# Kernel tuning notes

Measured on AMD Instinct MI355X. Metric: run time of the kernel, lower is better.

Reference implementation:

```python
import jax, jax.numpy as jnp
import numpy as np

B, S, HIDDEN = 2, 2048, 1024
NUM_HEADS, HEAD_DIM = 16, 64
STRIDE = 128
NEG = -10000.0


def _strided_mask(seq_len):
    # Sparse Transformer strided pattern: causal, local window of STRIDE,
    # plus every STRIDE-th previous position.
    i = jnp.arange(seq_len)[:, None]
    j = jnp.arange(seq_len)[None, :]
    diff = i - j
    allowed = (diff >= 0) & ((diff < STRIDE) | (diff % STRIDE == 0))
    return jnp.where(allowed, 0.0, NEG).astype(jnp.float32)  # [S, S]


def setup_inputs() -> dict:
    key = jax.random.key(0)
    k0, k1, k2, k3, k4 = jax.random.split(key, 5)
    hidden_states = jax.random.normal(k0, (B, S, HIDDEN), dtype=jnp.float32)
    attention_mask = jnp.zeros((B, 1, 1, S), dtype=jnp.float32)
    W_q = jax.random.normal(k1, (HIDDEN, HIDDEN), dtype=jnp.float32) * 0.02
    b_q = jnp.zeros((HIDDEN,), dtype=jnp.float32)
    W_v = jax.random.normal(k2, (HIDDEN, HIDDEN), dtype=jnp.float32) * 0.02
    b_v = jnp.zeros((HIDDEN,), dtype=jnp.float32)
    return {"hidden_states": hidden_states, "attention_mask": attention_mask,
            "W_q": W_q, "b_q": b_q, "W_v": W_v, "b_v": b_v}


def _heads(x):
    b, s, _ = x.shape
    return x.reshape(b, s, NUM_HEADS, HEAD_DIM).transpose(0, 2, 1, 3)  # [B,H,S,d]


def reference(hidden_states, attention_mask, W_q, b_q, W_v, b_v):
    q = _heads(hidden_states @ W_q + b_q)  # [B,H,S,d]
    v = _heads(hidden_states @ W_v + b_v)  # [B,H,S,d]
    hash_mask = _strided_mask(q.shape[-2])  # [S,S], broadcast over B,H
    # NB: source computes matmul(query, query^T) -- Q used for both sides.
    scores = jnp.einsum('bhid,bhjd->bhij', q, q) + hash_mask
    scores = scores / jnp.sqrt(jnp.asarray(HEAD_DIM, scores.dtype))
    scores = scores + attention_mask
    probs = jax.nn.softmax(scores, axis=-1)  # dropout p=0 (eval)
    ctx = jnp.einsum('bhij,bhjd->bhid', probs, v)  # [B,H,S,d]
    b = ctx.shape[0]
    return ctx.transpose(0, 2, 1, 3).reshape(b, -1, NUM_HEADS * HEAD_DIM)
```

## Files before the change

### kernel.cpp

```cpp
#include <hip/hip_runtime.h>

typedef __attribute__((ext_vector_type(8))) short short8;
typedef __attribute__((ext_vector_type(4))) float float4v;

__device__ inline float bf2f(ushort u) {
    unsigned v = ((unsigned)u) << 16;
    return __builtin_bit_cast(float, v);
}
__device__ inline ushort f2bf(float f) {
    unsigned u = __builtin_bit_cast(unsigned, f);
    u += 0x7FFFu + ((u >> 16) & 1u);
    return (ushort)(u >> 16);
}

__device__ inline void gload_lds16(const ushort* g, ushort* l) {
    __builtin_amdgcn_global_load_lds(
        (const __attribute__((address_space(1))) unsigned int*)g,
        (__attribute__((address_space(3))) unsigned int*)l,
        16, 0, 0);
}

__global__ __launch_bounds__(256) void prep(
    const float* __restrict__ hs, ushort* __restrict__ hsb,
    const float* __restrict__ Wq, const float* __restrict__ Wv,
    ushort* __restrict__ Wt) {
    __shared__ ushort tile[64][68];
    if (blockIdx.x < 1024) {
        const size_t base = ((size_t)blockIdx.x * 256 + threadIdx.x) * 16;
        union { ushort u[16]; uint4 v[2]; } o;
#pragma unroll
        for (int q = 0; q < 4; ++q) {
            float4v f = *(const float4v*)(hs + base + q * 4);
#pragma unroll
            for (int j = 0; j < 4; ++j) o.u[q * 4 + j] = f2bf(f[j]);
        }
        *(uint4*)(hsb + base)     = o.v[0];
        *(uint4*)(hsb + base + 8) = o.v[1];
        return;
    }
    const int idx = blockIdx.x - 1024;
    const int z = idx >> 8, yy = (idx >> 4) & 15, xx = idx & 15;
    const float* W = z ? Wv : Wq;
    ushort* Wto    = Wt + (z ? (size_t)1024 * 1024 : 0);
    const int k0 = yy * 64, n0 = xx * 64;
    const int tid = threadIdx.x;
    const int rr = tid >> 4;
    const int cc = (tid & 15) * 4;
    union U4 { ushort u[4]; uint2 v; };
#pragma unroll
    for (int i = 0; i < 4; ++i) {
        int row = rr + i * 16;
        float4v f = *(const float4v*)(W + (size_t)(k0 + row) * 1024 + n0 + cc);
        U4 x;
#pragma unroll
        for (int j = 0; j < 4; ++j) x.u[j] = f2bf(f[j]);
        *(uint2*)&tile[row][cc] = x.v;
    }
    __syncthreads();
#pragma unroll
    for (int i = 0; i < 4; ++i) {
        int row = rr + i * 16;
        U4 o;
#pragma unroll
        for (int j = 0; j < 4; ++j) o.u[j] = tile[cc + j][row];
        *(uint2*)(Wto + (size_t)(n0 + row) * 1024 + k0 + cc) = o.v;
    }
}

__global__ __launch_bounds__(512, 2) void qv_gemm(
    const ushort* __restrict__ hsb, const ushort* __restrict__ Wt,
    const float* __restrict__ bq, const float* __restrict__ bv,
    ushort* __restrict__ q_ws, ushort* __restrict__ v_ws) {
    __shared__ ushort smem[73728];
    const int wg = blockIdx.x;
    const int n0 = (wg & 7) * 256;
    const int m0 = (wg >> 3) * 128;
    const int tid  = threadIdx.x;
    const int wid  = tid >> 6, lane = tid & 63;
    const int quad = lane >> 4, l16 = lane & 15;
    const int wm = (wid >> 2) * 64;
    const int wn = (wid & 3) * 64;
    const int srow8 = tid >> 3;
    const int scb   = (tid & 7) * 16;

    auto stage = [&](int ktt, int bi, int r) {
        if (r < 2) {
            int row = r * 64 + srow8;
            int sb  = scb ^ ((row & 7) << 4);
            gload_lds16(hsb + (size_t)(m0 + row) * 1024 + ktt * 64 + (sb >> 1),
                        (ushort*)((char*)smem + bi * 49152 + r * 8192 + wid * 1024));
        } else {
            int row = (r - 2) * 64 + srow8;
            int sb  = scb ^ ((row & 7) << 4);
            gload_lds16(Wt + (size_t)(n0 + row) * 1024 + ktt * 64 + (sb >> 1),
                        (ushort*)((char*)smem + bi * 49152 + 16384 + (r - 2) * 8192 + wid * 1024));
        }
    };

    float4v acc[4][4] = {};

#pragma unroll
    for (int r = 0; r < 6; ++r) stage(0, 0, r);
#pragma unroll
    for (int r = 0; r < 6; ++r) stage(1, 1, r);

    int bi = 0;
    for (int ktt = 0; ktt < 16; ++ktt) {
        const char* Ab = (const char*)smem + bi * 49152;
        const char* Bb = Ab + 16384;

        if (ktt < 15) asm volatile("s_waitcnt vmcnt(6)" ::: "memory");
        else          asm volatile("s_waitcnt vmcnt(0)" ::: "memory");
        __builtin_amdgcn_s_barrier();
        __builtin_amdgcn_sched_barrier(0);

        short8 af[4][2], bfr[4][2];
#pragma unroll
        for (int mt = 0; mt < 4; ++mt) {
            int ar = wm + mt * 16 + l16;
            int sw = (ar & 7) << 4;
            af[mt][0] = *(const short8*)(Ab + ar * 128 + ((quad * 16) ^ sw));
        }
#pragma unroll
        for (int nt = 0; nt < 4; ++nt) {
            int br = wn + nt * 16 + l16;
            int sw = (br & 7) << 4;
            bfr[nt][0] = *(const short8*)(Bb + br * 128 + ((quad * 16) ^ sw));
        }
        __builtin_amdgcn_sched_barrier(0);
        const int kn = ktt + 2;
        const int b2 = (bi + 2 >= 3) ? bi - 1 : bi + 2;
        if (kn < 16) {
            stage(kn, b2, 0); stage(kn, b2, 1); stage(kn, b2, 2);
            stage(kn, b2, 3); stage(kn, b2, 4); stage(kn, b2, 5);
        }
#pragma unroll
        for (int mt = 0; mt < 4; ++mt) {
            int ar = wm + mt * 16 + l16;
            int sw = (ar & 7) << 4;
            af[mt][1] = *(const short8*)(Ab + ar * 128 + (((4 + quad) * 16) ^ sw));
        }
#pragma unroll
        for (int nt = 0; nt < 4; ++nt) {
            int br = wn + nt * 16 + l16;
            int sw = (br & 7) << 4;
            bfr[nt][1] = *(const short8*)(Bb + br * 128 + (((4 + quad) * 16) ^ sw));
        }
        __builtin_amdgcn_sched_barrier(0);
        asm volatile("s_waitcnt lgkmcnt(8)" ::: "memory");
        __builtin_amdgcn_sched_barrier(0);
        __builtin_amdgcn_s_setprio(1);
#pragma unroll
        for (int mt = 0; mt < 4; ++mt)
#pragma unroll
            for (int nt = 0; nt < 4; ++nt)
                acc[mt][nt] = __builtin_amdgcn_mfma_f32_16x16x32_bf16(
                    af[mt][0], bfr[nt][0], acc[mt][nt], 0, 0, 0);
        __builtin_amdgcn_s_setprio(0);
        asm volatile("s_waitcnt lgkmcnt(0)" ::: "memory");
        __builtin_amdgcn_sched_barrier(0);
        __builtin_amdgcn_s_setprio(1);
#pragma unroll
        for (int mt = 0; mt < 4; ++mt)
#pragma unroll
            for (int nt = 0; nt < 4; ++nt)
                acc[mt][nt] = __builtin_amdgcn_mfma_f32_16x16x32_bf16(
                    af[mt][1], bfr[nt][1], acc[mt][nt], 0, 0, 0);
        __builtin_amdgcn_s_setprio(0);

        bi = (bi + 1 >= 3) ? 0 : bi + 1;
    }

#pragma unroll
    for (int mt = 0; mt < 4; ++mt) {
#pragma unroll
        for (int nt = 0; nt < 4; ++nt) {
            int coln = n0 + wn + nt * 16 + l16;
            bool isq = coln < 1024;
            int c2 = isq ? coln : coln - 1024;
            float bsv = isq ? bq[c2] : bv[c2];
            ushort* outp = isq ? q_ws : v_ws;
            int hh = c2 >> 6, dd = c2 & 63;
#pragma unroll
            for (int reg = 0; reg < 4; ++reg) {
                int r = m0 + wm + mt * 16 + quad * 4 + reg;
                int bb = r >> 11, s = r & 2047;
                outp[(((size_t)bb * 16 + hh) * 2048 + s) * 64 + dd] =
                    f2bf(acc[mt][nt][reg] + bsv);
            }
        }
    }
}

#define SISSUE(As, Bs, Ms, idx) { const ushort* kr_ = q_ws + srbase + ((size_t)(idx) << 13); \
    As = *(const uint4*)kr_; Bs = *(const uint4*)(kr_ + 8); Ms = amask[amrow + ((idx) << 7)]; }
#define SCONS(As, Bs, Ms, kk) { union { uint4 v; ushort u[8]; } t0_, t1_; t0_.v = As; t1_.v = Bs; \
    float p_ = 0.f; \
    _Pragma("unroll") for (int jj = 0; jj < 8; ++jj) p_ += qv[jj] * bf2f(t0_.u[jj]); \
    _Pragma("unroll") for (int jj = 0; jj < 8; ++jj) p_ += qv[8 + jj] * bf2f(t1_.u[jj]); \
    p_ += __shfl_xor(p_, 1); p_ += __shfl_xor(p_, 2); \
    if ((tid & 3) == 0) Sstr[sr][kk] = p_ * 0.125f + Ms; }
#define VISSUE(As, Bs, idx) { const ushort* vr_ = v_ws + srbase + ((size_t)(idx) << 13); \
    As = *(const uint4*)vr_; Bs = *(const uint4*)(vr_ + 8); }
#define VCONS(As, Bs, kk) { float p_ = Sstr[sr][kk]; union { uint4 v; ushort u[8]; } t0_, t1_; \
    t0_.v = As; t1_.v = Bs; \
    _Pragma("unroll") for (int jj = 0; jj < 8; ++jj) acc16[jj] += p_ * bf2f(t0_.u[jj]); \
    _Pragma("unroll") for (int jj = 0; jj < 8; ++jj) acc16[8 + jj] += p_ * bf2f(t1_.u[jj]); }

__global__ __launch_bounds__(512, 4) void attn(
    const ushort* __restrict__ q_ws, const ushort* __restrict__ v_ws,
    const float* __restrict__ amask, float* __restrict__ out) {
    const int wg = blockIdx.x;
    const int lane8 = wg & 7;
    const int k8    = wg >> 3;
    const int kk    = k8 & 31, khalf = k8 >> 5;
    const int t  = khalf ? (15 - (kk & 15)) : (kk & 15);
    const int gq = (kk >> 4) + 2 * khalf;
    const int g  = gq * 8 + lane8;
    const int b  = g >> 4;
    const int h  = g & 15;

    __shared__ ushort KwPl[16384];
    __shared__ ushort VtS[16384];
    __shared__ float  Sstr[128][17];
    __shared__ float  amw[256];

    const int tid = threadIdx.x;
    const int wid = tid >> 6, lane = tid & 63;
    const int quad = lane >> 4, l16 = lane & 15;
    const int r0 = wid * 16;
    const size_t qbase = ((size_t)b * 16 + h) * 2048 * 64;
    const int base_row = (t - 1) * 128;
    const int nk = (t >= 2) ? (t - 1) : 0;

    const int sr = tid >> 2;
    const int dq = (tid & 3) * 16;
    const size_t srbase = qbase + (size_t)sr * 64 + dq;
    const size_t amrow  = (size_t)b * 2048 + sr;

#pragma unroll
    for (int i = 0; i < 4; ++i) {
        int u = tid + i * 512;
        int row = u >> 3, c = u & 7;
        int jg = base_row + row; if (jg < 0) jg = 0;
        int sc = c ^ (row & 7);
        gload_lds16(q_ws + qbase + (size_t)jg * 64 + sc * 8, &KwPl[u * 8]);
    }
    __builtin_amdgcn_sched_barrier(0);

    {
        const int vj = tid & 255, dh0 = (tid >> 8) * 32;
        int vjg = base_row + vj; if (vjg < 0) vjg = 0;
        const ushort* vsrc = v_ws + qbase + (size_t)vjg * 64 + dh0;
        int cj = vj >> 3, j7 = vj & 7;
#pragma unroll
        for (int d0 = 0; d0 < 32; d0 += 8) {
            union { uint4 v; ushort u[8]; } tmp;
            tmp.v = *(const uint4*)(vsrc + d0);
#pragma unroll
            for (int jj = 0; jj < 8; ++jj) {
                int dd = dh0 + d0 + jj;
                VtS[dd * 256 + ((cj ^ (dd & 7)) * 8) + j7] = tmp.u[jj];
            }
        }
        int amj = base_row + (tid & 255); if (amj < 0) amj = 0;
        amw[tid & 255] = amask[(size_t)b * 2048 + amj];
    }

    uint4 kA0{}, kB0{}, kA1{}, kB1{}, kA2{}, kB2{};
    float am0 = 0.f, am1 = 0.f, am2 = 0.f;
    if (nk > 0) {
        SISSUE(kA0, kB0, am0, 0);
        SISSUE(kA1, kB1, am1, (1 < nk ? 1 : 0));
        SISSUE(kA2, kB2, am2, (2 < nk ? 2 : 0));
    }

    asm volatile("s_waitcnt vmcnt(0) lgkmcnt(0)" ::: "memory");
    __builtin_amdgcn_s_barrier();
    __builtin_amdgcn_sched_barrier(0);

    if (nk > 0) {
        float qv[16];
#pragma unroll
        for (int cc = 0; cc < 2; ++cc) {
            int c = (dq >> 3) + cc;
            union { uint4 v; ushort u[8]; } tm;
            tm.v = *(const uint4*)&KwPl[(128 + sr) * 64 + ((c ^ (sr & 7)) * 8)];
#pragma unroll
            for (int jj = 0; jj < 8; ++jj) qv[cc * 8 + jj] = bf2f(tm.u[jj]);
        }
        for (int k = 0; k < nk; k += 3) {
            SCONS(kA0, kB0, am0, k);
            if (k + 3 < nk) SISSUE(kA0, kB0, am0, k + 3);
            if (k + 1 < nk) {
                SCONS(kA1, kB1, am1, k + 1);
                if (k + 4 < nk) SISSUE(kA1, kB1, am1, k + 4);
            }
            if (k + 2 < nk) {
                SCONS(kA2, kB2, am2, k + 2);
                if (k + 5 < nk) SISSUE(kA2, kB2, am2, k + 5);
            }
        }
    }

    float4v sacc[16] = {};
    __builtin_amdgcn_s_setprio(1);
#pragma unroll
    for (int ks = 0; ks < 2; ++ks) {
        int c = ks * 4 + quad;
        int sw = (c ^ (l16 & 7)) * 8;
        short8 af = *(const short8*)&KwPl[(128 + r0 + l16) * 64 + sw];
#pragma unroll
        for (int nt = 0; nt < 16; ++nt) {
            short8 bfr = *(const short8*)&KwPl[(nt * 16 + l16) * 64 + sw];
            sacc[nt] = __builtin_amdgcn_mfma_f32_16x16x32_bf16(af, bfr, sacc[nt], 0, 0, 0);
        }
    }
    __builtin_amdgcn_s_setprio(0);
    __syncthreads();

    unsigned pb[4][4];
#pragma unroll
    for (int reg = 0; reg < 4; ++reg) {
        int rr = r0 + quad * 4 + reg;
        float sstr_v = (l16 < nk) ? Sstr[rr][l16] : -INFINITY;
        float m = sstr_v;
#pragma unroll
        for (int nt = 0; nt < 16; ++nt) {
            int c = nt * 16 + l16;
            bool allowed = (c >= rr) && (c <= rr + 128) && (t > 0 || c >= 128);
            float x = allowed ? sacc[nt][reg] * 0.125f + amw[c] : -INFINITY;
            sacc[nt][reg] = x;
            m = fmaxf(m, x);
        }
#pragma unroll
        for (int off = 1; off < 16; off <<= 1) m = fmaxf(m, __shfl_xor(m, off));

        float es = (l16 < nk) ? __expf(sstr_v - m) : 0.f;
        float sum = es;
#pragma unroll
        for (int nt = 0; nt < 16; ++nt) {
            float x = sacc[nt][reg];
            float e = (x == -INFINITY) ? 0.f : __expf(x - m);
            sacc[nt][reg] = e; sum += e;
        }
#pragma unroll
        for (int off = 1; off < 16; off <<= 1) sum += __shfl_xor(sum, off);
        float rden = 1.f / sum;
#pragma unroll
        for (int nt = 0; nt < 8; ++nt) {
            int c = nt * 2 + (l16 >> 3);
            KwPl[rr * 128 + ((c ^ (rr & 15)) * 8) + (l16 & 7)] = f2bf(sacc[nt][reg] * rden);
        }
#pragma unroll
        for (int i2 = 0; i2 < 4; ++i2) {
            unsigned lo = f2bf(sacc[8 + 2 * i2][reg] * rden);
            unsigned hi = f2bf(sacc[9 + 2 * i2][reg] * rden);
            pb[reg][i2] = lo | (hi << 16);
        }
        if (l16 < nk) Sstr[rr][l16] = es * rden;
    }
    __syncthreads();

    uint4 vA0{}, vB0{}, vA1{}, vB1{}, vA2{}, vB2{};
    if (nk > 0) {
        VISSUE(vA0, vB0, 0);
        VISSUE(vA1, vB1, (1 < nk ? 1 : 0));
        VISSUE(vA2, vB2, (2 < nk ? 2 : 0));
    }

    float4v cacc[4] = {};
    __builtin_amdgcn_s_setprio(1);
#pragma unroll
    for (int ks = 0; ks < 4; ++ks) {
        int cp = ks * 4 + quad;
        short8 af = *(const short8*)&KwPl[(r0 + l16) * 128 + ((cp ^ l16) * 8)];
#pragma unroll
        for (int nt = 0; nt < 4; ++nt) {
            int sw = (cp ^ (l16 & 7)) * 8;
            short8 bfr = *(const short8*)&VtS[(nt * 16 + l16) * 256 + sw];
            cacc[nt] = __builtin_amdgcn_mfma_f32_16x16x32_bf16(af, bfr, cacc[nt], 0, 0, 0);
        }
    }
    __builtin_amdgcn_s_setprio(0);
    __syncthreads();

#pragma unroll
    for (int reg = 0; reg < 4; ++reg) {
        int rr = r0 + quad * 4 + reg;
#pragma unroll
        for (int i2 = 0; i2 < 4; ++i2) {
            int nt0 = 8 + 2 * i2;
#pragma unroll
            for (int e2 = 0; e2 < 2; ++e2) {
                int nt = nt0 + e2;
                int c = (nt - 8) * 2 + (l16 >> 3);
                ushort val = (ushort)((pb[reg][i2] >> (16 * e2)) & 0xFFFF);
                KwPl[rr * 128 + ((c ^ (rr & 15)) * 8) + (l16 & 7)] = val;
            }
        }
    }
    __syncthreads();

    __builtin_amdgcn_s_setprio(1);
#pragma unroll
    for (int ks = 0; ks < 4; ++ks) {
        int cp = ks * 4 + quad;
        short8 af = *(const short8*)&KwPl[(r0 + l16) * 128 + ((cp ^ l16) * 8)];
#pragma unroll
        for (int nt = 0; nt < 4; ++nt) {
            int cv = 16 + cp;
            int sw = (cv ^ (l16 & 7)) * 8;
            short8 bfr = *(const short8*)&VtS[(nt * 16 + l16) * 256 + sw];
            cacc[nt] = __builtin_amdgcn_mfma_f32_16x16x32_bf16(af, bfr, cacc[nt], 0, 0, 0);
        }
    }
    __builtin_amdgcn_s_setprio(0);

    float acc16[16] = {};
    if (nk > 0) {
        for (int k = 0; k < nk; k += 3) {
            VCONS(vA0, vB0, k);
            if (k + 3 < nk) VISSUE(vA0, vB0, k + 3);
            if (k + 1 < nk) {
                VCONS(vA1, vB1, k + 1);
                if (k + 4 < nk) VISSUE(vA1, vB1, k + 4);
            }
            if (k + 2 < nk) {
                VCONS(vA2, vB2, k + 2);
                if (k + 5 < nk) VISSUE(vA2, vB2, k + 5);
            }
        }
    }
    __syncthreads();

    float* ctxp = (float*)&VtS[0];
#pragma unroll
    for (int d4 = 0; d4 < 4; ++d4) {
        int c = (dq >> 2) + d4;
        *(float4v*)&ctxp[sr * 64 + ((c ^ (sr & 15)) * 4)] =
            *(const float4v*)&acc16[d4 * 4];
    }
    __syncthreads();

    const size_t obase = ((size_t)b * 2048 + (size_t)t * 128) * 1024 + (size_t)h * 64;
#pragma unroll
    for (int nt = 0; nt < 4; ++nt)
#pragma unroll
        for (int reg = 0; reg < 4; ++reg) {
            int rr = r0 + quad * 4 + reg;
            int d = nt * 16 + l16;
            float cstr = ctxp[rr * 64 + (((d >> 2) ^ (rr & 15)) * 4) + (d & 3)];
            out[obase + (size_t)rr * 1024 + d] = cacc[nt][reg] + cstr;
        }
}

extern "C" void kernel_launch(void* const* d_in, const int* in_sizes, int n_in,
                              void* d_out, int out_size, void* d_ws, size_t ws_size,
                              hipStream_t stream) {
    int ihs = -1, iam = -1, iw1 = -1, iw2 = -1, ib1 = -1, ib2 = -1;
    for (int i = 0; i < n_in; ++i) {
        int s = in_sizes[i];
        if      (s == 4194304) { if (ihs < 0) ihs = i; }
        else if (s == 4096)    { if (iam < 0) iam = i; }
        else if (s == 1048576) { if (iw1 < 0) iw1 = i; else if (iw2 < 0) iw2 = i; }
        else if (s == 1024)    { if (ib1 < 0) ib1 = i; else if (ib2 < 0) ib2 = i; }
    }
    if (ihs < 0) ihs = 0; if (iam < 0) iam = 1;
    if (iw1 < 0) iw1 = 2; if (ib1 < 0) ib1 = 3;
    if (iw2 < 0) iw2 = 4; if (ib2 < 0) ib2 = 5;

    const float* hs    = (const float*)d_in[ihs];
    const float* amask = (const float*)d_in[iam];
    const float* Wq    = (const float*)d_in[iw1];
    const float* bq    = (const float*)d_in[ib1];
    const float* Wv    = (const float*)d_in[iw2];
    const float* bv    = (const float*)d_in[ib2];
    float* out = (float*)d_out;

    char* ws = (char*)d_ws;
    ushort* Wt   = (ushort*)(ws);
    ushort* hsb  = (ushort*)(ws + (1u << 22));
    ushort* q_ws = (ushort*)(ws + (1u << 22) + (1u << 23));
    ushort* v_ws = (ushort*)(ws + (1u << 22) + (2u << 23));

    prep<<<1536, 256, 0, stream>>>(hs, hsb, Wq, Wv, Wt);
    qv_gemm<<<256, 512, 0, stream>>>(hsb, Wt, bq, bv, q_ws, v_ws);
    attn<<<512, 512, 0, stream>>>(q_ws, v_ws, amask, out);
}
```

Before: 131.7 us.

## Split strided-attention part into separate kernel with partial softmax merge

Moves the strided (every-128th) key contributions out of the main attention kernel into a new sattn kernel. That kernel computes a per-row max, sum and unnormalized context for the strided keys from LDS-staged Q/V, and writes them to workspace. The main kernel then merges these partials with its local-window softmax using the combined max and a rescale factor. This removes the serial, latency-bound strided loop from the MFMA kernel and balances work across blocks. In exchange it adds an extra launch and a round trip of float context through global memory.

```diff
diff --git a/kernel.cpp b/kernel.cpp
--- a/kernel.cpp
+++ b/kernel.cpp
@@ -192,24 +192,104 @@
     }
 }
 
-#define SISSUE(As, Bs, Ms, idx) { const ushort* kr_ = q_ws + srbase + ((size_t)(idx) << 13); \
-    As = *(const uint4*)kr_; Bs = *(const uint4*)(kr_ + 8); Ms = amask[amrow + ((idx) << 7)]; }
-#define SCONS(As, Bs, Ms, kk) { union { uint4 v; ushort u[8]; } t0_, t1_; t0_.v = As; t1_.v = Bs; \
-    float p_ = 0.f; \
-    _Pragma("unroll") for (int jj = 0; jj < 8; ++jj) p_ += qv[jj] * bf2f(t0_.u[jj]); \
-    _Pragma("unroll") for (int jj = 0; jj < 8; ++jj) p_ += qv[8 + jj] * bf2f(t1_.u[jj]); \
-    p_ += __shfl_xor(p_, 1); p_ += __shfl_xor(p_, 2); \
-    if ((tid & 3) == 0) Sstr[sr][kk] = p_ * 0.125f + Ms; }
-#define VISSUE(As, Bs, idx) { const ushort* vr_ = v_ws + srbase + ((size_t)(idx) << 13); \
-    As = *(const uint4*)vr_; Bs = *(const uint4*)(vr_ + 8); }
-#define VCONS(As, Bs, kk) { float p_ = Sstr[sr][kk]; union { uint4 v; ushort u[8]; } t0_, t1_; \
-    t0_.v = As; t1_.v = Bs; \
-    _Pragma("unroll") for (int jj = 0; jj < 8; ++jj) acc16[jj] += p_ * bf2f(t0_.u[jj]); \
-    _Pragma("unroll") for (int jj = 0; jj < 8; ++jj) acc16[8 + jj] += p_ * bf2f(t1_.u[jj]); }
+__global__ __launch_bounds__(512, 4) void sattn(
+    const ushort* __restrict__ q_ws, const ushort* __restrict__ v_ws,
+    const float* __restrict__ amask, float* __restrict__ ctx_s,
+    float* __restrict__ msss) {
+    __shared__ ushort Qs[16][16][72];
+    __shared__ ushort Vs[16][16][72];
+    __shared__ float  am[16][16];
+    const int wg = blockIdx.x;
+    const int rg = wg & 7;
+    const int g  = wg >> 3;
+    const int b  = g >> 4;
+    const int tid = threadIdx.x;
+    const size_t gh = (size_t)g * 2048 * 64;
+    const int r0g = rg * 16;
+
+    {
+        int row = tid >> 1, half = tid & 1;
+        int m = row >> 4, res = row & 15;
+        int j = m * 128 + r0g + res;
+        const ushort* qsrc = q_ws + gh + (size_t)j * 64 + half * 32;
+        const ushort* vsrc = v_ws + gh + (size_t)j * 64 + half * 32;
+#pragma unroll
+        for (int c = 0; c < 4; ++c) {
+            *(uint4*)&Qs[m][res][half * 32 + c * 8] = *(const uint4*)(qsrc + c * 8);
+            *(uint4*)&Vs[m][res][half * 32 + c * 8] = *(const uint4*)(vsrc + c * 8);
+        }
+        if (tid < 256)
+            am[tid >> 4][tid & 15] =
+                amask[(size_t)b * 2048 + (tid >> 4) * 128 + r0g + (tid & 15)];
+    }
+    __syncthreads();
+
+    const int ti  = tid >> 5;
+    const int res = (tid >> 1) & 15;
+    const int dh  = tid & 1, d0 = dh * 32;
+    const int cnt = (ti >= 2) ? (ti - 1) : 0;
+
+    float q[32];
+#pragma unroll
+    for (int c = 0; c < 4; ++c) {
+        union { uint4 v; ushort u[8]; } tm;
+        tm.v = *(const uint4*)&Qs[ti][res][d0 + c * 8];
+#pragma unroll
+        for (int jj = 0; jj < 8; ++jj) q[c * 8 + jj] = bf2f(tm.u[jj]);
+    }
+
+    float m = -INFINITY;
+    for (int k = 0; k < cnt; ++k) {
+        float p = 0.f;
+#pragma unroll
+        for (int c = 0; c < 4; ++c) {
+            union { uint4 v; ushort u[8]; } tm;
+            tm.v = *(const uint4*)&Qs[k][res][d0 + c * 8];
+#pragma unroll
+            for (int jj = 0; jj < 8; ++jj) p += q[c * 8 + jj] * bf2f(tm.u[jj]);
+        }
+        p += __shfl_xor(p, 1);
+        m = fmaxf(m, p * 0.125f + am[k][res]);
+    }
+
+    float sum = 0.f;
+    float ctx[32] = {};
+    for (int k = 0; k < cnt; ++k) {
+        float p = 0.f;
+#pragma unroll
+        for (int c = 0; c < 4; ++c) {
+            union { uint4 v; ushort u[8]; } tm;
+            tm.v = *(const uint4*)&Qs[k][res][d0 + c * 8];
+#pragma unroll
+            for (int jj = 0; jj < 8; ++jj) p += q[c * 8 + jj] * bf2f(tm.u[jj]);
+        }
+        p += __shfl_xor(p, 1);
+        float e = __expf(p * 0.125f + am[k][res] - m);
+        sum += e;
+#pragma unroll
+        for (int c = 0; c < 4; ++c) {
+            union { uint4 v; ushort u[8]; } tv;
+            tv.v = *(const uint4*)&Vs[k][res][d0 + c * 8];
+#pragma unroll
+            for (int jj = 0; jj < 8; ++jj) ctx[c * 8 + jj] += e * bf2f(tv.u[jj]);
+        }
+    }
+
+    if (cnt > 0) {
+        int i = ti * 128 + r0g + res;
+        size_t rb = (size_t)g * 2048 + i;
+        if (dh == 0) { msss[rb * 2] = m; msss[rb * 2 + 1] = sum; }
+        float* cp = ctx_s + rb * 64 + d0;
+#pragma unroll
+        for (int c = 0; c < 8; ++c)
+            *(float4v*)(cp + c * 4) = *(const float4v*)&ctx[c * 4];
+    }
+}
 
 __global__ __launch_bounds__(512, 4) void attn(
     const ushort* __restrict__ q_ws, const ushort* __restrict__ v_ws,
-    const float* __restrict__ amask, float* __restrict__ out) {
+    const float* __restrict__ amask, const float* __restrict__ ctx_s,
+    const float* __restrict__ msss, float* __restrict__ out) {
     const int wg = blockIdx.x;
     const int lane8 = wg & 7;
     const int k8    = wg >> 3;
@@ -218,25 +298,19 @@
     const int gq = (kk >> 4) + 2 * khalf;
     const int g  = gq * 8 + lane8;
     const int b  = g >> 4;
-    const int h  = g & 15;
 
     __shared__ ushort KwPl[16384];
     __shared__ ushort VtS[16384];
-    __shared__ float  Sstr[128][17];
     __shared__ float  amw[256];
+    __shared__ float  msl[128][2];
+    __shared__ float  fsw[128];
 
     const int tid = threadIdx.x;
     const int wid = tid >> 6, lane = tid & 63;
     const int quad = lane >> 4, l16 = lane & 15;
     const int r0 = wid * 16;
-    const size_t qbase = ((size_t)b * 16 + h) * 2048 * 64;
+    const size_t qbase = (size_t)g * 2048 * 64;
     const int base_row = (t - 1) * 128;
-    const int nk = (t >= 2) ? (t - 1) : 0;
-
-    const int sr = tid >> 2;
-    const int dq = (tid & 3) * 16;
-    const size_t srbase = qbase + (size_t)sr * 64 + dq;
-    const size_t amrow  = (size_t)b * 2048 + sr;
 
 #pragma unroll
     for (int i = 0; i < 4; ++i) {
@@ -265,43 +339,20 @@
         }
         int amj = base_row + (tid & 255); if (amj < 0) amj = 0;
         amw[tid & 255] = amask[(size_t)b * 2048 + amj];
-    }
-
-    uint4 kA0{}, kB0{}, kA1{}, kB1{}, kA2{}, kB2{};
-    float am0 = 0.f, am1 = 0.f, am2 = 0.f;
-    if (nk > 0) {
-        SISSUE(kA0, kB0, am0, 0);
-        SISSUE(kA1, kB1, am1, (1 < nk ? 1 : 0));
-        SISSUE(kA2, kB2, am2, (2 < nk ? 2 : 0));
+        if (tid < 128) {
+            if (t >= 2) {
+                size_t rb = (size_t)g * 2048 + t * 128 + tid;
+                msl[tid][0] = msss[rb * 2];
+                msl[tid][1] = msss[rb * 2 + 1];
+            } else {
+                msl[tid][0] = -INFINITY; msl[tid][1] = 0.f;
+            }
+        }
     }
 
     asm volatile("s_waitcnt vmcnt(0) lgkmcnt(0)" ::: "memory");
     __builtin_amdgcn_s_barrier();
     __builtin_amdgcn_sched_barrier(0);
-
-    if (nk > 0) {
-        float qv[16];
-#pragma unroll
-        for (int cc = 0; cc < 2; ++cc) {
-            int c = (dq >> 3) + cc;
-            union { uint4 v; ushort u[8]; } tm;
-            tm.v = *(const uint4*)&KwPl[(128 + sr) * 64 + ((c ^ (sr & 7)) * 8)];
-#pragma unroll
-            for (int jj = 0; jj < 8; ++jj) qv[cc * 8 + jj] = bf2f(tm.u[jj]);
-        }
-        for (int k = 0; k < nk; k += 3) {
-            SCONS(kA0, kB0, am0, k);
-            if (k + 3 < nk) SISSUE(kA0, kB0, am0, k + 3);
-            if (k + 1 < nk) {
-                SCONS(kA1, kB1, am1, k + 1);
-                if (k + 4 < nk) SISSUE(kA1, kB1, am1, k + 4);
-            }
-            if (k + 2 < nk) {
-                SCONS(kA2, kB2, am2, k + 2);
-                if (k + 5 < nk) SISSUE(kA2, kB2, am2, k + 5);
-            }
-        }
-    }
 
     float4v sacc[16] = {};
     __builtin_amdgcn_s_setprio(1);
@@ -323,8 +374,8 @@
 #pragma unroll
     for (int reg = 0; reg < 4; ++reg) {
         int rr = r0 + quad * 4 + reg;
-        float sstr_v = (l16 < nk) ? Sstr[rr][l16] : -INFINITY;
-        float m = sstr_v;
+        float msv = msl[rr][0], ssv = msl[rr][1];
+        float m = -INFINITY;
 #pragma unroll
         for (int nt = 0; nt < 16; ++nt) {
             int c = nt * 16 + l16;
@@ -335,18 +386,20 @@
         }
 #pragma unroll
         for (int off = 1; off < 16; off <<= 1) m = fmaxf(m, __shfl_xor(m, off));
-
-        float es = (l16 < nk) ? __expf(sstr_v - m) : 0.f;
-        float sum = es;
+        float M = fmaxf(m, msv);
+
+        float sum = 0.f;
 #pragma unroll
         for (int nt = 0; nt < 16; ++nt) {
             float x = sacc[nt][reg];
-            float e = (x == -INFINITY) ? 0.f : __expf(x - m);
+            float e = (x == -INFINITY) ? 0.f : __expf(x - M);
             sacc[nt][reg] = e; sum += e;
         }
 #pragma unroll
         for (int off = 1; off < 16; off <<= 1) sum += __shfl_xor(sum, off);
-        float rden = 1.f / sum;
+
+        float fs = (t >= 2) ? __expf(msv - M) : 0.f;
+        float rden = 1.f / (sum + ssv * fs);
 #pragma unroll
         for (int nt = 0; nt < 8; ++nt) {
             int c = nt * 2 + (l16 >> 3);
@@ -358,16 +411,9 @@
             unsigned hi = f2bf(sacc[9 + 2 * i2][reg] * rden);
             pb[reg][i2] = lo | (hi << 16);
         }
-        if (l16 < nk) Sstr[rr][l16] = es * rden;
+        if (l16 == 0) fsw[rr] = fs * rden;
     }
     __syncthreads();
-
-    uint4 vA0{}, vB0{}, vA1{}, vB1{}, vA2{}, vB2{};
-    if (nk > 0) {
-        VISSUE(vA0, vB0, 0);
-        VISSUE(vA1, vB1, (1 < nk ? 1 : 0));
-        VISSUE(vA2, vB2, (2 < nk ? 2 : 0));
-    }
 
     float4v cacc[4] = {};
     __builtin_amdgcn_s_setprio(1);
@@ -417,40 +463,16 @@
     }
     __builtin_amdgcn_s_setprio(0);
 
-    float acc16[16] = {};
-    if (nk > 0) {
-        for (int k = 0; k < nk; k += 3) {
-            VCONS(vA0, vB0, k);
-            if (k + 3 < nk) VISSUE(vA0, vB0, k + 3);
-            if (k + 1 < nk) {
-                VCONS(vA1, vB1, k + 1);
-                if (k + 4 < nk) VISSUE(vA1, vB1, k + 4);
-            }
-            if (k + 2 < nk) {
-                VCONS(vA2, vB2, k + 2);
-                if (k + 5 < nk) VISSUE(vA2, vB2, k + 5);
-            }
-        }
-    }
-    __syncthreads();
-
-    float* ctxp = (float*)&VtS[0];
-#pragma unroll
-    for (int d4 = 0; d4 < 4; ++d4) {
-        int c = (dq >> 2) + d4;
-        *(float4v*)&ctxp[sr * 64 + ((c ^ (sr & 15)) * 4)] =
-            *(const float4v*)&acc16[d4 * 4];
-    }
-    __syncthreads();
-
-    const size_t obase = ((size_t)b * 2048 + (size_t)t * 128) * 1024 + (size_t)h * 64;
+    const size_t obase = ((size_t)b * 2048 + (size_t)t * 128) * 1024 +
+                         (size_t)(g & 15) * 64;
+    const float* ctxrow = ctx_s + ((size_t)g * 2048 + (size_t)t * 128) * 64;
 #pragma unroll
     for (int nt = 0; nt < 4; ++nt)
 #pragma unroll
         for (int reg = 0; reg < 4; ++reg) {
             int rr = r0 + quad * 4 + reg;
             int d = nt * 16 + l16;
-            float cstr = ctxp[rr * 64 + (((d >> 2) ^ (rr & 15)) * 4) + (d & 3)];
+            float cstr = (t >= 2) ? ctxrow[(size_t)rr * 64 + d] * fsw[rr] : 0.f;
             out[obase + (size_t)rr * 1024 + d] = cacc[nt][reg] + cstr;
         }
 }
@@ -479,12 +501,15 @@
     float* out = (float*)d_out;
 
     char* ws = (char*)d_ws;
-    ushort* Wt   = (ushort*)(ws);
-    ushort* hsb  = (ushort*)(ws + (1u << 22));
-    ushort* q_ws = (ushort*)(ws + (1u << 22) + (1u << 23));
-    ushort* v_ws = (ushort*)(ws + (1u << 22) + (2u << 23));
+    ushort* Wt    = (ushort*)(ws);
+    ushort* hsb   = (ushort*)(ws + (1u << 22));
+    ushort* q_ws  = (ushort*)(ws + (1u << 22) + (1u << 23));
+    ushort* v_ws  = (ushort*)(ws + (1u << 22) + (2u << 23));
+    float*  ctx_s = (float*)(ws + (7u << 22));
+    float*  msss  = (float*)(ws + (11u << 22));
 
     prep<<<1536, 256, 0, stream>>>(hs, hsb, Wq, Wv, Wt);
     qv_gemm<<<256, 512, 0, stream>>>(hsb, Wt, bq, bv, q_ws, v_ws);
-    attn<<<512, 512, 0, stream>>>(q_ws, v_ws, amask, out);
-}
+    sattn<<<256, 512, 0, stream>>>(q_ws, v_ws, amask, ctx_s, msss);
+    attn<<<512, 512, 0, stream>>>(q_ws, v_ws, amask, ctx_s, msss, out);
+}
```

After: 137.6 us. 1.05x slower.
